# Performance work log

Hardware: AMD Instinct MI355X
Metric: run time of the kernel (lower is better)

The kernel has to match this reference:

```python
import jax, jax.numpy as jnp
import numpy as np

B, C, N, V, W, D = 4, 64, 8, 32, 32, 256  # spa_dim = D


def _ln(x, g, b, eps=1e-5):
    m = jnp.mean(x, -1, keepdims=True)
    v = jnp.mean((x - m) ** 2, -1, keepdims=True)
    return (x - m) * jax.lax.rsqrt(v + eps) * g + b


def _tokens(x):
    # (b, c, n, v, w) -> (b*n, v*w, c)
    b, c, n, v, w = x.shape
    return x.transpose(0, 2, 3, 4, 1).reshape(b * n, v * w, c)


def setup_inputs() -> dict:
    key = jax.random.key(0)
    ks = jax.random.split(key, 8)
    fea_lf = jax.random.normal(ks[0], (B, C, N, V, W), jnp.float32)
    fea_hf = jax.random.normal(ks[1], (B, C, N, V, W), jnp.float32)
    W_in = jax.random.normal(ks[2], (C, D), jnp.float32) / np.sqrt(C)
    W_kv = jax.random.normal(ks[3], (C, 2 * D), jnp.float32) / np.sqrt(C)
    gamma = jnp.ones((D,), jnp.float32)
    beta = jnp.zeros((D,), jnp.float32)
    g2 = jnp.ones((D,), jnp.float32)
    b2 = jnp.zeros((D,), jnp.float32)
    W1 = jax.random.normal(ks[4], (D, 2 * D), jnp.float32) / np.sqrt(D)
    W2 = jax.random.normal(ks[5], (2 * D, D), jnp.float32) / np.sqrt(2 * D)
    W_out = jax.random.normal(ks[6], (D, C), jnp.float32) / np.sqrt(D)
    return {"fea_lf": fea_lf, "fea_hf": fea_hf, "W_in": W_in, "W_kv": W_kv,
            "gamma": gamma, "beta": beta, "g2": g2, "b2": b2,
            "W1": W1, "W2": W2, "W_out": W_out}


def reference(fea_lf, fea_hf, W_in, W_kv, gamma, beta, g2, b2, W1, W2, W_out):
    b, c, n, v, w = fea_lf.shape
    S = v * w
    tok_q = _tokens(fea_lf)   # (bn, S, c)
    tok_kv = _tokens(fea_hf)  # (bn, S, c)
    q = _ln(tok_q @ W_in, gamma, beta)              # (bn, S, D)
    kv = tok_kv @ W_kv
    k, vtok = jnp.split(kv, 2, axis=-1)
    k = _ln(k, gamma, beta)                          # shared LayerNorm (self.norm)
    # NOTE: original has no 1/sqrt(d) scaling on scores.
    score = jnp.einsum('bqd,bkd->bqk', q, k)         # (bn, S, S)
    mask = jnp.tril(jnp.ones((S, S), bool))
    score = jnp.where(mask, score, jnp.float32(-1e15))
    p = jax.nn.softmax(score, axis=-1)
    att = jnp.einsum('bqk,bkd->bqd', p, vtok)        # (bn, S, D)
    h = jax.nn.relu(_ln(att, g2, b2) @ W1) @ W2      # FFN (dropout=0)
    epi = h + vtok
    out = epi @ W_out                                # (bn, S, c)
    return out.reshape(b, n, v, w, c).transpose(0, 4, 1, 2, 3)
```

## Files before the change

### kernel.cpp

```cpp
#include <hip/hip_runtime.h>

typedef short bf16x8 __attribute__((ext_vector_type(8)));
typedef _Float16 f16x8 __attribute__((ext_vector_type(8)));
typedef float f32x4 __attribute__((ext_vector_type(4)));
typedef unsigned short u16;
typedef unsigned short u16x4 __attribute__((ext_vector_type(4)));

#define MFMA(a, b, c) __builtin_amdgcn_mfma_f32_16x16x32_bf16(a, b, c, 0, 0, 0)
#define MFMAH(a, b, c) __builtin_amdgcn_mfma_f32_16x16x32_f16(a, b, c, 0, 0, 0)

__device__ __forceinline__ u16 f2b(float f) {
    union { float f; unsigned u; } x{f};
    unsigned r = (x.u + 0x7FFFu + ((x.u >> 16) & 1u)) >> 16;
    return (u16)r;
}
__device__ __forceinline__ float b2f(u16 h) {
    union { unsigned u; float f; } x{((unsigned)h) << 16};
    return x.f;
}
__device__ __forceinline__ u16 f2h(float f) {
    _Float16 h = (_Float16)f;
    return *reinterpret_cast<u16*>(&h);
}
__device__ __forceinline__ float h2f(u16 h) {
    _Float16 v = *reinterpret_cast<_Float16*>(&h);
    return (float)v;
}
__device__ __forceinline__ float red16_sum(float v) {
#pragma unroll
    for (int m = 1; m < 16; m <<= 1) v += __shfl_xor(v, m, 64);
    return v;
}
__device__ __forceinline__ float red16_max(float v) {
#pragma unroll
    for (int m = 1; m < 16; m <<= 1) v = fmaxf(v, __shfl_xor(v, m, 64));
    return v;
}
__device__ __forceinline__ void gl_lds16(const void* g, void* l) {
    __builtin_amdgcn_global_load_lds(
        (const __attribute__((address_space(1))) unsigned int*)(g),
        (__attribute__((address_space(3))) unsigned int*)(l), 16, 0, 0);
}


__global__ __launch_bounds__(256) void wconv_kernel(
    const float* __restrict__ W1, const float* __restrict__ W2,
    const float* __restrict__ Wo, const float* __restrict__ Win,
    const float* __restrict__ Wkv, u16* __restrict__ w1T,
    u16* __restrict__ w2T, u16* __restrict__ woT, u16* __restrict__ wfrag) {
    int id = blockIdx.x * 256 + threadIdx.x;
    if (id < 131072) {
        int n = id >> 8, k = id & 255;
        w1T[id] = f2b(W1[k * 512 + n]);
    } else if (id < 262144) {
        int j = id - 131072;
        int n = j >> 9, k = j & 511;
        w2T[j] = f2b(W2[k * 256 + n]);
    } else if (id < 278528) {
        int j = id - 262144;
        int n = j >> 8, k = j & 255;
        woT[j] = f2b(Wo[k * 64 + n]);
    } else if (id < 284672) {
        int fid = id - 278528;
        int arr = fid >> 11;
        int e = fid & 2047;
        int ntck = e >> 6, ln = e & 63;
        int lr = ln & 15, lg2 = ln >> 4;
        int nt = ntck >> 1, ck = ntck & 1;
        int d = nt * 16 + lr;
#pragma unroll
        for (int j = 0; j < 8; j++) {
            int c = ck * 32 + lg2 * 8 + j;
            float x;
            if (arr == 0)      x = Win[c * 256 + d];
            else if (arr == 1) x = Wkv[c * 512 + d];
            else               x = Wkv[c * 512 + 256 + d];
            wfrag[arr * 16384 + e * 8 + j] = f2h(x);
        }
    }
}

#define PJ_A 0
#define PJ_WREG 16384
#define PJ_WORK 49152
__global__ __launch_bounds__(512, 1) void proj_kernel(
    const float* __restrict__ lf, const float* __restrict__ hf,
    const u16* __restrict__ wqg, const u16* __restrict__ wkg,
    const u16* __restrict__ wvg, const float* __restrict__ gamma,
    const float* __restrict__ beta, u16* __restrict__ qf_,
    u16* __restrict__ kf_, u16* __restrict__ vT) {
    extern __shared__ char sm[];
    const int tid = threadIdx.x;
    const int wave = tid >> 6, lane = tid & 63, lr = lane & 15, lg = lane >> 4;
    const int st = blockIdx.x, bn = blockIdx.y;
    const int b = bn >> 3, n = bn & 7;
    const int s0 = st * 128;
    const size_t baseF = (size_t)b * 524288 + (size_t)n * 1024 + s0;

    float gam[16], bet[16];
#pragma unroll
    for (int nt = 0; nt < 16; nt++) {
        gam[nt] = gamma[nt * 16 + lr];
        bet[nt] = beta[nt * 16 + lr];
    }

    auto stage32 = [&](const float* srcbase, int chalf) {
#pragma unroll
        for (int call = 0; call < 2; call++) {
            int unit = call * 8 + wave;
            int obase = unit << 10;
            int e = unit * 256 + lane * 4;
            int cl = e >> 7, si = e & 127;
            gl_lds16(srcbase + (size_t)(chalf * 32 + cl) * 8192 + si,
                     sm + PJ_WORK + obase);
        }
    };
    auto stageW = [&](const u16* wsrc) {
#pragma unroll
        for (int call = 0; call < 4; call++) {
            int obase = (call * 8 + wave) << 10;
            gl_lds16((const char*)wsrc + obase + lane * 16, sm + PJ_WREG + obase);
        }
    };
    auto buildA = [&](int slotbase) {
        int g = wave >> 1;
        int s = ((wave & 1) << 6) | lane;
        float x[8];
#pragma unroll
        for (int cc = 0; cc < 8; cc++)
            x[cc] = *(const float*)(sm + PJ_WORK + ((g * 8 + cc) << 9) + (s << 2));
        f16x8 ph;
#pragma unroll
        for (int cc = 0; cc < 8; cc++) ph[cc] = (_Float16)x[cc];
        int slp = (slotbase + g) ^ (s & 7);
        *(f16x8*)(sm + PJ_A + (s << 7) + (slp << 4)) = ph;
    };
    auto loadA = [&](f16x8* aF) {
        int tl = wave * 16 + lr;
#pragma unroll
        for (int ck = 0; ck < 2; ck++) {
            int off = (tl << 7) + ((((ck << 2) | lg) ^ (tl & 7)) << 4);
            aF[ck] = *(const f16x8*)(sm + PJ_A + off);
        }
    };
    auto pass1 = [&](const f16x8* aF, f32x4* acc) {
#pragma unroll
        for (int nt = 0; nt < 16; nt++) acc[nt] = (f32x4){0.f, 0.f, 0.f, 0.f};
#pragma unroll
        for (int nt = 0; nt < 16; nt++) {
#pragma unroll
            for (int ck = 0; ck < 2; ck++) {
                int wo = (((nt << 1) | ck) << 10) + (lane << 4);
                f16x8 bh = *(const f16x8*)(sm + PJ_WREG + wo);
                acc[nt] = MFMAH(aF[ck], bh, acc[nt]);
            }
        }
    };
    auto lnstats = [&](const f32x4* acc, float* mean, float* rs) {
#pragma unroll
        for (int r = 0; r < 4; r++) {
            float s1 = 0.f, s2 = 0.f;
#pragma unroll
            for (int nt = 0; nt < 16; nt++) {
                float xv = acc[nt][r];
                s1 += xv; s2 += xv * xv;
            }
            s1 = red16_sum(s1);
            s2 = red16_sum(s2);
            float mn = s1 * (1.f / 256.f);
            float var = s2 * (1.f / 256.f) - mn * mn;
            mean[r] = mn;
            rs[r] = rsqrtf(var + 1e-5f);
        }
    };
    auto emit = [&](const f32x4* acc, const float* mean, const float* rs,
                    u16* dst) {
        char* bw = sm + ((wave < 4) ? (wave * 4096)
                                    : (PJ_WORK + (wave - 4) * 4096));
        const int gtok = bn * 1024 + s0 + wave * 16;
#pragma unroll
        for (int hh = 0; hh < 2; hh++) {
#pragma unroll
            for (int ntl = 0; ntl < 8; ntl++) {
                int nt = hh * 8 + ntl;
#pragma unroll
                for (int r = 0; r < 4; r++) {
                    float y = (acc[nt][r] - mean[r]) * rs[r] * gam[nt] + bet[nt];
                    int tl = lg * 4 + r;
                    int dl = ntl * 16 + lr;
                    int sl = dl >> 3;
                    *(u16*)(bw + tl * 256 + ((sl ^ ((tl >> 2) & 3)) << 4) +
                            (dl & 7) * 2) = f2h(y);
                }
            }
#pragma unroll
            for (int p = 0; p < 4; p++) {
                int row = lane >> 2, slq = (lane & 3) + p * 4;
                bf16x8 v8 = *(const bf16x8*)(bw + row * 256 +
                                             ((slq ^ ((row >> 2) & 3)) << 4));
                *(bf16x8*)(dst + (size_t)(gtok + row) * 256 + hh * 128 +
                           slq * 8) = v8;
            }
        }
    };

    f32x4 acc[16];
    float mean[4], rs[4];
    f16x8 aF[2];

    stage32(lf + baseF, 0);  __syncthreads();
    buildA(0);               __syncthreads();
    stage32(lf + baseF, 1);
    stageW(wqg);             __syncthreads();
    buildA(4);               __syncthreads();
    loadA(aF);
    pass1(aF, acc);
    lnstats(acc, mean, rs);  __syncthreads();
    stageW(wkg);
    emit(acc, mean, rs, qf_);
    __syncthreads();
    stage32(hf + baseF, 0);  __syncthreads();
    buildA(0);               __syncthreads();
    stage32(hf + baseF, 1);  __syncthreads();
    buildA(4);               __syncthreads();
    loadA(aF);
    pass1(aF, acc);
    lnstats(acc, mean, rs);  __syncthreads();
    stageW(wvg);
    emit(acc, mean, rs, kf_);
    __syncthreads();
    pass1(aF, acc);
#pragma unroll
    for (int nt = 0; nt < 16; nt++) {
        u16x4 pv;
#pragma unroll
        for (int r = 0; r < 4; r++) pv[r] = f2h(acc[nt][r]);
        *(u16x4*)(vT + ((size_t)(bn * 256) + nt * 16 + lr) * 1024 + s0 +
                  wave * 16 + lg * 4) = pv;
    }
}

__global__ __launch_bounds__(512) void attn_kernel(
    const u16* __restrict__ qf_, const u16* __restrict__ kf_,
    const u16* __restrict__ vT, const float* __restrict__ g2,
    const float* __restrict__ b2, u16* __restrict__ lnatt) {
    extern __shared__ char smem[];
    const int tid = threadIdx.x;
    const int wave = tid >> 6, lane = tid & 63, lr = lane & 15, lg = lane >> 4;
    const int grp = wave >> 2, w4 = wave & 3;
    const int b = blockIdx.x;
    const int bn = b & 31;
    const int strip = 15 - (b >> 5);
    const int qr0 = strip * 64 + w4 * 16;
    const int ni = strip + 1;
    const int ktbase = grp * ni;
    char* myK = smem + grp * 65536;
    char* myV = smem + grp * 65536 + 32768;
    u16* Pw = (u16*)(smem + 131072 + wave * 1280);

    f16x8 qf[8];
    {
        const size_t off = ((size_t)(bn * 1024 + qr0 + lr)) * 256 + lg * 8;
#pragma unroll
        for (int ck = 0; ck < 8; ck++)
            qf[ck] = *(const f16x8*)(qf_ + off + ck * 32);
    }
    f16x8 onesb;
    {
        _Float16 v1 = (lr == 0) ? (_Float16)1.0f : (_Float16)0.0f;
#pragma unroll
        for (int q = 0; q < 8; q++) onesb[q] = v1;
    }

    const int srl = lane >> 5, ss = lane & 31;
    const int vdl = lane >> 2, vg = lane & 3;
    auto stage = [&](int buf, int kt) {
        const int kv0 = kt << 5;
        char* baseK = myK + buf * 16384;
        char* baseV = myV + buf * 16384;
#pragma unroll
        for (int ii = 0; ii < 4; ii++) {
            int u = w4 * 4 + ii;
            int r = u * 2 + srl;
            size_t go = (((size_t)((bn << 10) + kv0 + r)) << 8) +
                        (unsigned)((ss ^ (r & 7)) << 3);
            gl_lds16(kf_ + go, baseK + u * 1024);
            int d = u * 16 + vdl;
            size_t gv = (((size_t)((bn << 8) + d)) << 10) + kv0 +
                        (unsigned)((vg ^ ((d >> 1) & 3)) << 3);
            gl_lds16(vT + gv, baseV + u * 1024);
        }
    };

    f32x4 o[16];
#pragma unroll
    for (int i = 0; i < 16; i++) o[i] = (f32x4){0.f, 0.f, 0.f, 0.f};
    f32x4 ol = (f32x4){0.f, 0.f, 0.f, 0.f};
    float m[4] = {-INFINITY, -INFINITY, -INFINITY, -INFINITY};

    stage(0, ktbase);
    for (int it = 0; it < ni; it++) {
        const int cur = it & 1;
        asm volatile("s_waitcnt vmcnt(0)" ::: "memory");
        __builtin_amdgcn_s_barrier();
        asm volatile("" ::: "memory");
        if (it + 1 < ni) stage(cur ^ 1, ktbase + it + 1);
        const int kt = ktbase + it;
        if ((kt << 5) <= qr0 + 15) {
            const char* kb = myK + cur * 16384;
            f32x4 sc0 = (f32x4){0.f, 0.f, 0.f, 0.f};
            f32x4 sc1 = (f32x4){0.f, 0.f, 0.f, 0.f};
            __builtin_amdgcn_s_setprio(1);
#pragma unroll
            for (int ck = 0; ck < 8; ck++) {
                int sw = ((ck * 4 + lg) ^ (lr & 7)) << 4;
                int a0 = lr * 512 + sw;
                f16x8 k0 = *(const f16x8*)(kb + a0);
                f16x8 k1 = *(const f16x8*)(kb + a0 + 8192);
                sc0 = MFMAH(qf[ck], k0, sc0);
                sc1 = MFMAH(qf[ck], k1, sc1);
            }
            __builtin_amdgcn_s_setprio(0);
            float scl[4];
            const int kvb = kt << 5;
#pragma unroll
            for (int r = 0; r < 4; r++) {
                int qi = qr0 + lg * 4 + r;
                float s0v = (kvb + lr > qi) ? -1e30f : sc0[r];
                float s1v = (kvb + 16 + lr > qi) ? -1e30f : sc1[r];
                float tm = red16_max(fmaxf(s0v, s1v));
                float mn = fmaxf(m[r], tm);
                scl[r] = __expf(m[r] - mn);
                m[r] = mn;
                int row = lg * 4 + r;
                Pw[row * 40 + lr] = f2h(__expf(s0v - mn));
                Pw[row * 40 + 16 + lr] = f2h(__expf(s1v - mn));
            }
#pragma unroll
            for (int f = 0; f < 16; f++) {
                f32x4 t = o[f];
                t[0] *= scl[0]; t[1] *= scl[1]; t[2] *= scl[2]; t[3] *= scl[3];
                o[f] = t;
            }
            ol[0] *= scl[0]; ol[1] *= scl[1]; ol[2] *= scl[2]; ol[3] *= scl[3];
            asm volatile("" ::: "memory");
            f16x8 pa = *(const f16x8*)((const char*)Pw + lr * 80 + lg * 16);
            const char* vb = myV + cur * 16384;
            __builtin_amdgcn_s_setprio(1);
#pragma unroll
            for (int db = 0; db < 16; db++) {
                int d = db * 16 + lr;
                f16x8 vf = *(const f16x8*)(vb + d * 64 +
                                           ((lg ^ ((lr >> 1) & 3)) << 4));
                o[db] = MFMAH(pa, vf, o[db]);
            }
            ol = MFMAH(pa, onesb, ol);
            __builtin_amdgcn_s_setprio(0);
        }
    }
    __syncthreads();
    float lsum[4];
#pragma unroll
    for (int r = 0; r < 4; r++) lsum[r] = __shfl(ol[r], lane & 48, 64);

    char* cb = smem + 65536;
    float* mlb = (float*)(smem + 131072);
    if (grp == 1) {
        char* po = cb + w4 * 16384;
#pragma unroll
        for (int f = 0; f < 16; f++)
            *(f32x4*)(po + (f * 16 + lr) * 64 + lg * 16) = o[f];
        if (lr == 0) {
#pragma unroll
            for (int r = 0; r < 4; r++) {
                int row = lg * 4 + r;
                mlb[(w4 * 16 + row) * 2] = m[r];
                mlb[(w4 * 16 + row) * 2 + 1] = lsum[r];
            }
        }
    }
    __syncthreads();
    if (grp == 0) {
        const char* po = cb + w4 * 16384;
        float e0[4], e1[4], linv[4];
#pragma unroll
        for (int r = 0; r < 4; r++) {
            int row = lg * 4 + r;
            float m1 = mlb[(w4 * 16 + row) * 2];
            float l1 = mlb[(w4 * 16 + row) * 2 + 1];
            float ms = fmaxf(m[r], m1);
            e0[r] = __expf(m[r] - ms);
            e1[r] = __expf(m1 - ms);
            linv[r] = 1.f / (lsum[r] * e0[r] + l1 * e1[r]);
        }
#pragma unroll
        for (int f = 0; f < 16; f++) {
            f32x4 o1 = *(const f32x4*)(po + (f * 16 + lr) * 64 + lg * 16);
#pragma unroll
            for (int r = 0; r < 4; r++)
                o[f][r] = (o[f][r] * e0[r] + o1[r] * e1[r]) * linv[r];
        }
        float gv[16], bv[16];
#pragma unroll
        for (int f = 0; f < 16; f++) {
            gv[f] = g2[f * 16 + lr];
            bv[f] = b2[f * 16 + lr];
        }
#pragma unroll
        for (int r = 0; r < 4; r++) {
            float s1 = 0.f, s2 = 0.f;
#pragma unroll
            for (int f = 0; f < 16; f++) {
                float x = o[f][r];
                s1 += x; s2 += x * x;
            }
            s1 = red16_sum(s1);
            s2 = red16_sum(s2);
            float mean = s1 * (1.f / 256.f);
            float var = s2 * (1.f / 256.f) - mean * mean;
            float rsv = rsqrtf(var + 1e-5f);
            size_t row = (size_t)(bn * 1024 + qr0 + lg * 4 + r) * 256;
#pragma unroll
            for (int f = 0; f < 16; f++)
                lnatt[row + f * 16 + lr] =
                    f2b((o[f][r] - mean) * rsv * gv[f] + bv[f]);
        }
    }
}

template <int K, int NB, int MODE>
__global__ __launch_bounds__(512) void gemmB_kernel(
    const u16* __restrict__ A, const u16* __restrict__ BT,
    u16* __restrict__ outb, const u16* __restrict__ vTr,
    float* __restrict__ outf, int ldOut) {
    extern __shared__ char bsm[];
    const int tid = threadIdx.x;
    const int wave = tid >> 6, lane = tid & 63, lr = lane & 15, lg = lane >> 4;
    constexpr int K2 = K * 2;
    constexpr int BN = NB * 16;
    constexpr int TILE = BN * K2;
    const int m0 = blockIdx.x * 128 + wave * 16;
    const int n0 = blockIdx.y * BN;
    {
        const char* bsrc = (const char*)(BT + (size_t)n0 * K);
        constexpr int ITER = TILE / (512 * 16);
#pragma unroll
        for (int it = 0; it < ITER; it++) {
            int o = (it * 512 + tid) * 16;
            int col = o / K2;
            int slot = (o % K2) >> 4;
            int src = col * K2 + ((slot ^ (col & 7)) << 4);
            gl_lds16(bsrc + src, bsm + o);
        }
    }
    __syncthreads();
    f32x4 acc[NB];
#pragma unroll
    for (int nb = 0; nb < NB; nb++) acc[nb] = (f32x4){0.f, 0.f, 0.f, 0.f};
    const u16* ap = A + (size_t)(m0 + lr) * K + lg * 8;
#pragma unroll
    for (int kc = 0; kc < K; kc += 32) {
        bf16x8 a = *(const bf16x8*)(ap + kc);
        int ks = (kc >> 3) + lg;
#pragma unroll
        for (int nb = 0; nb < NB; nb++) {
            int c = nb * 16 + lr;
            bf16x8 bv = *(const bf16x8*)(bsm + c * K2 + ((ks ^ (c & 7)) << 4));
            acc[nb] = MFMA(a, bv, acc[nb]);
        }
    }
    const int g = m0 + lg * 4;
    if (MODE == 0) {
#pragma unroll
        for (int nb = 0; nb < NB; nb++)
#pragma unroll
            for (int r = 0; r < 4; r++)
                outb[(size_t)(g + r) * ldOut + n0 + nb * 16 + lr] =
                    f2b(fmaxf(acc[nb][r], 0.f));
    } else if (MODE == 1) {
        int bn = g >> 10, s = g & 1023;
#pragma unroll
        for (int nb = 0; nb < NB; nb++) {
            int dd = n0 + nb * 16 + lr;
            u16x4 vv = *(const u16x4*)(vTr + ((size_t)bn * 256 + dd) * 1024 + s);
#pragma unroll
            for (int r = 0; r < 4; r++)
                outb[(size_t)(g + r) * 256 + dd] = f2b(acc[nb][r] + h2f(vv[r]));
        }
    } else {
        int bn = g >> 10, s = g & 1023;
        int bb = bn >> 3, nn = bn & 7;
#pragma unroll
        for (int nb = 0; nb < NB; nb++) {
            int cc = n0 + nb * 16 + lr;
            *(f32x4*)(outf + (size_t)bb * 524288 + (size_t)cc * 8192 +
                      (size_t)nn * 1024 + s) = acc[nb];
        }
    }
}

extern "C" void kernel_launch(void* const* d_in, const int* in_sizes, int n_in,
                              void* d_out, int out_size, void* d_ws, size_t ws_size,
                              hipStream_t stream) {
    const float* lf    = (const float*)d_in[0];
    const float* hf    = (const float*)d_in[1];
    const float* Win   = (const float*)d_in[2];
    const float* Wkv   = (const float*)d_in[3];
    const float* gamma = (const float*)d_in[4];
    const float* beta  = (const float*)d_in[5];
    const float* g2    = (const float*)d_in[6];
    const float* b2    = (const float*)d_in[7];
    const float* W1    = (const float*)d_in[8];
    const float* W2    = (const float*)d_in[9];
    const float* Wo    = (const float*)d_in[10];
    float* out = (float*)d_out;

    char* w = (char*)d_ws;
    const size_t MB16 = 16777216;
    u16* qf  = (u16*)(w);
    u16* kf  = (u16*)(w + MB16);
    u16* vT  = (u16*)(w + 2 * MB16);
    u16* hb  = (u16*)(w + 3 * MB16);
    u16* w1T = (u16*)(w + 3 * MB16 + 33554432);
    u16* w2T = w1T + 131072;
    u16* woT = w2T + 131072;
    u16* wfrag = woT + 16384;
    u16* wqg = wfrag;
    u16* wkg = wfrag + 16384;
    u16* wvg = wfrag + 32768;
    u16* lnatt = qf;
    u16* epib  = kf;

    wconv_kernel<<<dim3(1136), dim3(256), 0, stream>>>(W1, W2, Wo, Win, Wkv,
                                                       w1T, w2T, woT, wfrag);
    proj_kernel<<<dim3(8, 32), dim3(512), 65536, stream>>>(
        lf, hf, wqg, wkg, wvg, gamma, beta, qf, kf, vT);
    attn_kernel<<<dim3(512), dim3(512), 141312, stream>>>(qf, kf, vT, g2, b2,
                                                          lnatt);
    gemmB_kernel<256, 8, 0><<<dim3(256, 4), dim3(512), 65536, stream>>>(
        lnatt, w1T, hb, nullptr, nullptr, 512);
    gemmB_kernel<512, 8, 1><<<dim3(256, 2), dim3(512), 131072, stream>>>(
        hb, w2T, epib, vT, nullptr, 256);
    gemmB_kernel<256, 4, 2><<<dim3(256, 1), dim3(512), 32768, stream>>>(
        epib, woT, nullptr, nullptr, out, 64);
}
```

Measured before the change: 128.7 us.

## Drop intra-block split-KV in attention; one 4-wave group per block

Previously the attention kernel ran 8 waves per block as two groups, each covering half the causal KV range, and merged their partial softmax states through shared memory. Now each block has 4 waves that walk the whole KV range alone, so the merge and its extra barriers go away and shared memory per block is halved. Strips are reordered so that the heavy ones are dispatched first, then the light ones. The cost is a serial KV loop up to twice as long per block, in exchange for possibly fitting two blocks per CU.

```diff
diff --git a/kernel.cpp b/kernel.cpp
--- a/kernel.cpp
+++ b/kernel.cpp
@@ -240,23 +240,22 @@
     }
 }
 
-__global__ __launch_bounds__(512) void attn_kernel(
+__global__ __launch_bounds__(256) void attn_kernel(
     const u16* __restrict__ qf_, const u16* __restrict__ kf_,
     const u16* __restrict__ vT, const float* __restrict__ g2,
     const float* __restrict__ b2, u16* __restrict__ lnatt) {
     extern __shared__ char smem[];
     const int tid = threadIdx.x;
     const int wave = tid >> 6, lane = tid & 63, lr = lane & 15, lg = lane >> 4;
-    const int grp = wave >> 2, w4 = wave & 3;
     const int b = blockIdx.x;
     const int bn = b & 31;
-    const int strip = 15 - (b >> 5);
-    const int qr0 = strip * 64 + w4 * 16;
-    const int ni = strip + 1;
-    const int ktbase = grp * ni;
-    char* myK = smem + grp * 65536;
-    char* myV = smem + grp * 65536 + 32768;
-    u16* Pw = (u16*)(smem + 131072 + wave * 1280);
+    const int g = b >> 5;
+    const int strip = (g < 8) ? (15 - g) : (g - 8);
+    const int qr0 = strip * 64 + wave * 16;
+    const int ni = 2 * strip + 2;
+    char* myK = smem;
+    char* myV = smem + 32768;
+    u16* Pw = (u16*)(smem + 65536 + wave * 1280);
 
     f16x8 qf[8];
     {
@@ -280,7 +279,7 @@
         char* baseV = myV + buf * 16384;
 #pragma unroll
         for (int ii = 0; ii < 4; ii++) {
-            int u = w4 * 4 + ii;
+            int u = wave * 4 + ii;
             int r = u * 2 + srl;
             size_t go = (((size_t)((bn << 10) + kv0 + r)) << 8) +
                         (unsigned)((ss ^ (r & 7)) << 3);
@@ -298,15 +297,14 @@
     f32x4 ol = (f32x4){0.f, 0.f, 0.f, 0.f};
     float m[4] = {-INFINITY, -INFINITY, -INFINITY, -INFINITY};
 
-    stage(0, ktbase);
+    stage(0, 0);
     for (int it = 0; it < ni; it++) {
         const int cur = it & 1;
         asm volatile("s_waitcnt vmcnt(0)" ::: "memory");
         __builtin_amdgcn_s_barrier();
         asm volatile("" ::: "memory");
-        if (it + 1 < ni) stage(cur ^ 1, ktbase + it + 1);
-        const int kt = ktbase + it;
-        if ((kt << 5) <= qr0 + 15) {
+        if (it + 1 < ni) stage(cur ^ 1, it + 1);
+        if ((it << 5) <= qr0 + 15) {
             const char* kb = myK + cur * 16384;
             f32x4 sc0 = (f32x4){0.f, 0.f, 0.f, 0.f};
             f32x4 sc1 = (f32x4){0.f, 0.f, 0.f, 0.f};
@@ -322,7 +320,7 @@
             }
             __builtin_amdgcn_s_setprio(0);
             float scl[4];
-            const int kvb = kt << 5;
+            const int kvb = it << 5;
 #pragma unroll
             for (int r = 0; r < 4; r++) {
                 int qi = qr0 + lg * 4 + r;
@@ -358,73 +356,34 @@
             __builtin_amdgcn_s_setprio(0);
         }
     }
-    __syncthreads();
-    float lsum[4];
-#pragma unroll
-    for (int r = 0; r < 4; r++) lsum[r] = __shfl(ol[r], lane & 48, 64);
-
-    char* cb = smem + 65536;
-    float* mlb = (float*)(smem + 131072);
-    if (grp == 1) {
-        char* po = cb + w4 * 16384;
+    float linv[4];
+#pragma unroll
+    for (int r = 0; r < 4; r++) linv[r] = 1.f / __shfl(ol[r], lane & 48, 64);
+#pragma unroll
+    for (int f = 0; f < 16; f++) {
+        o[f][0] *= linv[0]; o[f][1] *= linv[1];
+        o[f][2] *= linv[2]; o[f][3] *= linv[3];
+    }
+    float gv[16], bv[16];
+#pragma unroll
+    for (int f = 0; f < 16; f++) {
+        gv[f] = g2[f * 16 + lr];
+        bv[f] = b2[f * 16 + lr];
+    }
+#pragma unroll
+    for (int r = 0; r < 4; r++) {
+        float s1 = 0.f, s2 = 0.f;
+#pragma unroll
+        for (int f = 0; f < 16; f++) { float x = o[f][r]; s1 += x; s2 += x * x; }
+        s1 = red16_sum(s1);
+        s2 = red16_sum(s2);
+        float mean = s1 * (1.f / 256.f);
+        float var = s2 * (1.f / 256.f) - mean * mean;
+        float rsv = rsqrtf(var + 1e-5f);
+        size_t row = (size_t)(bn * 1024 + qr0 + lg * 4 + r) * 256;
 #pragma unroll
         for (int f = 0; f < 16; f++)
-            *(f32x4*)(po + (f * 16 + lr) * 64 + lg * 16) = o[f];
-        if (lr == 0) {
-#pragma unroll
-            for (int r = 0; r < 4; r++) {
-                int row = lg * 4 + r;
-                mlb[(w4 * 16 + row) * 2] = m[r];
-                mlb[(w4 * 16 + row) * 2 + 1] = lsum[r];
-            }
-        }
-    }
-    __syncthreads();
-    if (grp == 0) {
-        const char* po = cb + w4 * 16384;
-        float e0[4], e1[4], linv[4];
-#pragma unroll
-        for (int r = 0; r < 4; r++) {
-            int row = lg * 4 + r;
-            float m1 = mlb[(w4 * 16 + row) * 2];
-            float l1 = mlb[(w4 * 16 + row) * 2 + 1];
-            float ms = fmaxf(m[r], m1);
-            e0[r] = __expf(m[r] - ms);
-            e1[r] = __expf(m1 - ms);
-            linv[r] = 1.f / (lsum[r] * e0[r] + l1 * e1[r]);
-        }
-#pragma unroll
-        for (int f = 0; f < 16; f++) {
-            f32x4 o1 = *(const f32x4*)(po + (f * 16 + lr) * 64 + lg * 16);
-#pragma unroll
-            for (int r = 0; r < 4; r++)
-                o[f][r] = (o[f][r] * e0[r] + o1[r] * e1[r]) * linv[r];
-        }
-        float gv[16], bv[16];
-#pragma unroll
-        for (int f = 0; f < 16; f++) {
-            gv[f] = g2[f * 16 + lr];
-            bv[f] = b2[f * 16 + lr];
-        }
-#pragma unroll
-        for (int r = 0; r < 4; r++) {
-            float s1 = 0.f, s2 = 0.f;
-#pragma unroll
-            for (int f = 0; f < 16; f++) {
-                float x = o[f][r];
-                s1 += x; s2 += x * x;
-            }
-            s1 = red16_sum(s1);
-            s2 = red16_sum(s2);
-            float mean = s1 * (1.f / 256.f);
-            float var = s2 * (1.f / 256.f) - mean * mean;
-            float rsv = rsqrtf(var + 1e-5f);
-            size_t row = (size_t)(bn * 1024 + qr0 + lg * 4 + r) * 256;
-#pragma unroll
-            for (int f = 0; f < 16; f++)
-                lnatt[row + f * 16 + lr] =
-                    f2b((o[f][r] - mean) * rsv * gv[f] + bv[f]);
-        }
+            lnatt[row + f * 16 + lr] = f2b((o[f][r] - mean) * rsv * gv[f] + bv[f]);
     }
 }
 
@@ -535,8 +494,8 @@
                                                        w1T, w2T, woT, wfrag);
     proj_kernel<<<dim3(8, 32), dim3(512), 65536, stream>>>(
         lf, hf, wqg, wkg, wvg, gamma, beta, qf, kf, vT);
-    attn_kernel<<<dim3(512), dim3(512), 141312, stream>>>(qf, kf, vT, g2, b2,
-                                                          lnatt);
+    attn_kernel<<<dim3(512), dim3(256), 70656, stream>>>(qf, kf, vT, g2, b2,
+                                                         lnatt);
     gemmB_kernel<256, 8, 0><<<dim3(256, 4), dim3(512), 65536, stream>>>(
         lnatt, w1T, hb, nullptr, nullptr, 512);
     gemmB_kernel<512, 8, 1><<<dim3(256, 2), dim3(512), 131072, stream>>>(
```

After: 140.2 us. 1.09x slower.
